# Optimization experiments

Hardware: AMD Instinct MI355X
Metric: run time of the kernel (lower is better)

The kernel has to match this reference:

```python
import jax, jax.numpy as jnp
import numpy as np

NUM_HEADS = 16
NEG_INF = -1e30


def setup_inputs() -> dict:
    key = jax.random.key(0)
    k1, k2, k3 = jax.random.split(key, 3)
    B, S, D = 2, 2048, 1024
    x = jax.random.normal(k1, (B, S, D), dtype=jnp.float32)
    # torch Linear(D, 3D, bias=False) stored here already transposed: y = x @ w_qkv
    w_qkv = jax.random.normal(k2, (D, 3 * D), dtype=jnp.float32) * 0.02
    w_out = jax.random.normal(k3, (D, D), dtype=jnp.float32) * 0.02
    return {"x": x, "w_qkv": w_qkv, "w_out": w_out}


def reference(x, w_qkv, w_out):
    B, S, D = x.shape
    H = NUM_HEADS
    dh = D // H
    qkv = x @ w_qkv                      # [B, S, 3D]
    q, k, v = jnp.split(qkv, 3, axis=-1)

    def to_heads(t):
        return t.reshape(B, S, H, dh).transpose(0, 2, 1, 3)  # [B, H, S, dh]

    q, k, v = to_heads(q), to_heads(k), to_heads(v)
    scale = jnp.asarray(dh, x.dtype) ** -0.5
    scores = jnp.einsum('bhqd,bhkd->bhqk', q, k) * scale     # [B, H, S, S]
    causal = jnp.tril(jnp.ones((S, S), dtype=bool))
    scores = jnp.where(causal, scores, NEG_INF)
    attn = jax.nn.softmax(scores, axis=-1)
    out = jnp.einsum('bhqk,bhkd->bhqd', attn, v)             # [B, H, S, dh]
    out = out.transpose(0, 2, 1, 3).reshape(B, S, D)
    return out @ w_out
```

## Files before the change

kernel.cpp:

```cpp
#include <hip/hip_runtime.h>

typedef unsigned short u16;
typedef unsigned int u32;

typedef __bf16 bf16x8 __attribute__((ext_vector_type(8)));
typedef _Float16 f16x8 __attribute__((ext_vector_type(8)));
typedef _Float16 f16x2 __attribute__((ext_vector_type(2)));
typedef float f32x4 __attribute__((ext_vector_type(4)));

typedef __attribute__((address_space(1))) u32 as1_u32;
typedef __attribute__((address_space(3))) u32 as3_u32;

__device__ __forceinline__ u16 f2bf(float x) {
  u32 u = __float_as_uint(x);
  u = u + 0x7fffu + ((u >> 16) & 1u);
  return (u16)(u >> 16);
}
__device__ __forceinline__ u32 pack2(float a, float b) {
  return (u32)f2bf(a) | ((u32)f2bf(b) << 16);
}
__device__ __forceinline__ u32 pkf16(float a, float b) {
  return __builtin_bit_cast(u32, __builtin_amdgcn_cvt_pkrtz(a, b));
}
__device__ __forceinline__ void gld_lds16(const u16* g, const u16* l) {
  __builtin_amdgcn_global_load_lds((const as1_u32*)g, (as3_u32*)l, 16, 0, 0);
}

__global__ void cvt_bf16_kernel(const float* __restrict__ in, u16* __restrict__ out, int n4) {
  int i = blockIdx.x * blockDim.x + threadIdx.x;
  if (i < n4) {
    float4 v = ((const float4*)in)[i];
    uint2 r;
    r.x = pack2(v.x, v.y);
    r.y = pack2(v.z, v.w);
    ((uint2*)out)[i] = r;
  }
}

__global__ __launch_bounds__(256) void transpose_bf16_tiled(const float* __restrict__ W,
                                                            u16* __restrict__ WT,
                                                            int K, int N) {
  __shared__ float tile[64][65];
  int k0 = blockIdx.x * 64, n0 = blockIdx.y * 64;
  int t = threadIdx.x;
  int r = t >> 4, c4 = (t & 15) * 4;
#pragma unroll
  for (int i = 0; i < 4; ++i) {
    int row = r + i * 16;
    float4 v = *(const float4*)&W[(size_t)(k0 + row) * N + n0 + c4];
    tile[row][c4 + 0] = v.x; tile[row][c4 + 1] = v.y;
    tile[row][c4 + 2] = v.z; tile[row][c4 + 3] = v.w;
  }
  __syncthreads();
#pragma unroll
  for (int i = 0; i < 4; ++i) {
    int n = r + i * 16;
    uint2 o;
    o.x = pack2(tile[c4 + 0][n], tile[c4 + 1][n]);
    o.y = pack2(tile[c4 + 2][n], tile[c4 + 3][n]);
    *(uint2*)&WT[(size_t)(n0 + n) * K + k0 + c4] = o;
  }
}

template <int OUT_MODE>
__global__ __launch_bounds__(256) void gemm_bt_kernel(const u16* __restrict__ A,
                                                      const u16* __restrict__ BT,
                                                      void* __restrict__ Cv,
                                                      u16* __restrict__ VT,
                                                      int M, int N, int K) {
  __shared__ __attribute__((aligned(16))) u16 sA[128 * 32];
  __shared__ __attribute__((aligned(16))) u16 sB[128 * 32];
  const int tid = threadIdx.x;
  const int wave = tid >> 6;
  const int lane = tid & 63;
  const int bm = blockIdx.y * 128;
  const int bn = blockIdx.x * 128;
  const int wm = (wave >> 1) * 64;
  const int wn = (wave & 1) * 64;
  const int lr = lane & 15;
  const int kg = lane >> 4;

  const int srow = tid >> 2;
  const int scol = (tid & 3) * 8;
  const u16* pa0 = A + (size_t)(bm + srow) * K + scol;
  const u16* pa1 = pa0 + (size_t)64 * K;
  const u16* pb0 = BT + (size_t)(bn + srow) * K + scol;
  const u16* pb1 = pb0 + (size_t)64 * K;
  const u16* la = sA + wave * 512;
  const u16* lb = sB + wave * 512;

  f32x4 acc[4][4];
#pragma unroll
  for (int i = 0; i < 4; i++)
#pragma unroll
    for (int j = 0; j < 4; j++) {
      f32x4 z = {0.f, 0.f, 0.f, 0.f};
      acc[i][j] = z;
    }

  for (int k0 = 0; k0 < K; k0 += 32) {
    __syncthreads();
    gld_lds16(pa0 + k0, la);
    gld_lds16(pa1 + k0, la + 2048);
    gld_lds16(pb0 + k0, lb);
    gld_lds16(pb1 + k0, lb + 2048);
    __syncthreads();
    bf16x8 af[4], bfr[4];
#pragma unroll
    for (int mi = 0; mi < 4; mi++)
      af[mi] = *(const bf16x8*)(sA + (wm + mi * 16 + lr) * 32 + kg * 8);
#pragma unroll
    for (int ni = 0; ni < 4; ni++)
      bfr[ni] = *(const bf16x8*)(sB + (wn + ni * 16 + lr) * 32 + kg * 8);
#pragma unroll
    for (int mi = 0; mi < 4; mi++)
#pragma unroll
      for (int ni = 0; ni < 4; ni++)
        acc[mi][ni] = __builtin_amdgcn_mfma_f32_16x16x32_bf16(af[mi], bfr[ni], acc[mi][ni], 0, 0, 0);
  }

#pragma unroll
  for (int mi = 0; mi < 4; mi++)
#pragma unroll
    for (int ni = 0; ni < 4; ni++) {
      int c = bn + wn + ni * 16 + lr;
      int r0 = bm + wm + mi * 16 + kg * 4;
      if (OUT_MODE == 0) {
#pragma unroll
        for (int rr = 0; rr < 4; rr++)
          ((float*)Cv)[(size_t)(r0 + rr) * N + c] = acc[mi][ni][rr];
      } else {
        if (c < 2048) {
          u16* qkp = (u16*)Cv;
#pragma unroll
          for (int rr = 0; rr < 4; rr++)
            qkp[(size_t)(r0 + rr) * 2048 + c] = f2bf(acc[mi][ni][rr]);
        } else {
          int cc = c - 2048;
          u32 lo = pkf16(acc[mi][ni][0], acc[mi][ni][1]);
          u32 hi = pkf16(acc[mi][ni][2], acc[mi][ni][3]);
          size_t vrow = ((size_t)(r0 >> 11) * 16 + (cc >> 6)) * 64 + (cc & 63);
          *(uint2*)(VT + vrow * 2048 + (r0 & 2047)) = make_uint2(lo, hi);
        }
      }
    }
}

__global__ __launch_bounds__(256) void attn_mfma_kernel(const u16* __restrict__ qk,
                                                        const u16* __restrict__ vt,
                                                        u16* __restrict__ out) {
  __shared__ __attribute__((aligned(16))) u16 sQ[2][64 * 32];
  __shared__ __attribute__((aligned(16))) u16 sK[2][64 * 32];
  __shared__ __attribute__((aligned(16))) u16 sV[2][64 * 32];
  __shared__ __attribute__((aligned(16))) u16 sP[4][16 * 72];

  const int tid = threadIdx.x;
  const int wave = tid >> 6;
  const int lane = tid & 63;
  const int lq = lane & 15;
  const int lg = lane >> 4;

  int idx = blockIdx.x;
  int qc = 31 - (idx >> 5);
  int bh = idx & 31;
  int b = bh >> 4, h = bh & 15;
  int q0 = qc * 64;

  const u16* qbase = qk + (size_t)b * 2048 * 2048 + h * 64;
  const u16* kbase = qbase + 1024;
  const u16* vbase = vt + (size_t)(b * 16 + h) * 64 * 2048;
  u16* obase = out + (size_t)b * 2048 * 1024 + h * 64;

  const int sreg = wave >> 1;
  const int srb = wave & 1;

#pragma unroll
  for (int it = 0; it < 2; ++it) {
    int rows0 = (srb * 2 + it) * 16;
    int row = rows0 + (lane >> 2);
    gld_lds16(qbase + (size_t)(q0 + row) * 2048 + sreg * 32 + (lane & 3) * 8,
              sQ[sreg] + rows0 * 32);
  }
  __syncthreads();

  bf16x8 qf0 = *(const bf16x8*)(sQ[0] + (wave * 16 + lq) * 32 + lg * 8);
  bf16x8 qf1 = *(const bf16x8*)(sQ[1] + (wave * 16 + lq) * 32 + lg * 8);

  float lsum = 0.f;
  f32x4 oacc[4];
#pragma unroll
  for (int i = 0; i < 4; ++i) {
    f32x4 z = {0.f, 0.f, 0.f, 0.f};
    oacc[i] = z;
  }

  const float EK = 0.18033688011112042f;
  u16* const pw = sP[wave] + lq * 72 + lg * 4;
  const u16* const pr = sP[wave] + lq * 72 + lg * 8;

  const int ntiles = qc + 1;
  for (int t = 0; t < ntiles; ++t) {
    int j0 = t * 64;
    __syncthreads();
#pragma unroll
    for (int it = 0; it < 2; ++it) {
      int rows0 = (srb * 2 + it) * 16;
      int row = rows0 + (lane >> 2);
      int coff = sreg * 32 + (lane & 3) * 8;
      gld_lds16(kbase + (size_t)(j0 + row) * 2048 + coff, sK[sreg] + rows0 * 32);
      gld_lds16(vbase + (size_t)row * 2048 + j0 + coff, sV[sreg] + rows0 * 32);
    }
    __syncthreads();

    if (t < qc) {
#pragma unroll
      for (int jt = 0; jt < 4; ++jt) {
        bf16x8 kf0 = *(const bf16x8*)(sK[0] + (jt * 16 + lq) * 32 + lg * 8);
        bf16x8 kf1 = *(const bf16x8*)(sK[1] + (jt * 16 + lq) * 32 + lg * 8);
        f32x4 c = {0.f, 0.f, 0.f, 0.f};
        c = __builtin_amdgcn_mfma_f32_16x16x32_bf16(kf0, qf0, c, 0, 0, 0);
        c = __builtin_amdgcn_mfma_f32_16x16x32_bf16(kf1, qf1, c, 0, 0, 0);
        float p0 = exp2f(c[0] * EK);
        float p1 = exp2f(c[1] * EK);
        float p2 = exp2f(c[2] * EK);
        float p3 = exp2f(c[3] * EK);
        lsum += (p0 + p1) + (p2 + p3);
        *(uint2*)(pw + jt * 16) = make_uint2(pkf16(p0, p1), pkf16(p2, p3));
      }
    } else {
#pragma unroll
      for (int jt = 0; jt < 4; ++jt) {
        if (jt <= wave) {
          bf16x8 kf0 = *(const bf16x8*)(sK[0] + (jt * 16 + lq) * 32 + lg * 8);
          bf16x8 kf1 = *(const bf16x8*)(sK[1] + (jt * 16 + lq) * 32 + lg * 8);
          f32x4 c = {0.f, 0.f, 0.f, 0.f};
          c = __builtin_amdgcn_mfma_f32_16x16x32_bf16(kf0, qf0, c, 0, 0, 0);
          c = __builtin_amdgcn_mfma_f32_16x16x32_bf16(kf1, qf1, c, 0, 0, 0);
          float p0 = exp2f(c[0] * EK);
          float p1 = exp2f(c[1] * EK);
          float p2 = exp2f(c[2] * EK);
          float p3 = exp2f(c[3] * EK);
          if (jt == wave) {
            int jr = lg * 4;
            p0 = (jr + 0 <= lq) ? p0 : 0.f;
            p1 = (jr + 1 <= lq) ? p1 : 0.f;
            p2 = (jr + 2 <= lq) ? p2 : 0.f;
            p3 = (jr + 3 <= lq) ? p3 : 0.f;
          }
          lsum += (p0 + p1) + (p2 + p3);
          *(uint2*)(pw + jt * 16) = make_uint2(pkf16(p0, p1), pkf16(p2, p3));
        } else {
          *(uint2*)(pw + jt * 16) = make_uint2(0u, 0u);
        }
      }
    }

    asm volatile("" ::: "memory");

    f16x8 pf0 = *(const f16x8*)(pr);
    f16x8 pf1 = *(const f16x8*)(pr + 32);
#pragma unroll
    for (int dt = 0; dt < 4; ++dt) {
      f16x8 vf0 = *(const f16x8*)(sV[0] + (dt * 16 + lq) * 32 + lg * 8);
      f16x8 vf1 = *(const f16x8*)(sV[1] + (dt * 16 + lq) * 32 + lg * 8);
      oacc[dt] = __builtin_amdgcn_mfma_f32_16x16x32_f16(vf0, pf0, oacc[dt], 0, 0, 0);
      oacc[dt] = __builtin_amdgcn_mfma_f32_16x16x32_f16(vf1, pf1, oacc[dt], 0, 0, 0);
    }
  }

  lsum += __shfl_xor(lsum, 16);
  lsum += __shfl_xor(lsum, 32);
  float inv = 1.0f / lsum;

#pragma unroll
  for (int dt = 0; dt < 4; ++dt) {
    int d = dt * 16 + lg * 4;
    u32 lo = pack2(oacc[dt][0] * inv, oacc[dt][1] * inv);
    u32 hi = pack2(oacc[dt][2] * inv, oacc[dt][3] * inv);
    *(uint2*)(obase + (size_t)(q0 + wave * 16 + lq) * 1024 + d) = make_uint2(lo, hi);
  }
}

extern "C" void kernel_launch(void* const* d_in, const int* in_sizes, int n_in,
                              void* d_out, int out_size, void* d_ws, size_t ws_size,
                              hipStream_t stream) {
  const float* x = (const float*)d_in[0];
  const float* w_qkv = (const float*)d_in[1];
  const float* w_out = (const float*)d_in[2];
  float* out = (float*)d_out;

  char* ws = (char*)d_ws;
  u16* xb    = (u16*)(ws);
  u16* wqkvT = (u16*)(ws + (8u << 20));
  u16* woutT = (u16*)(ws + (14u << 20));
  u16* qkb   = (u16*)(ws + (16u << 20));
  u16* vtb   = (u16*)(ws + (32u << 20));
  u16* attn  = (u16*)(ws + (40u << 20));

  cvt_bf16_kernel<<<4096, 256, 0, stream>>>(x, xb, 4194304 / 4);
  transpose_bf16_tiled<<<dim3(16, 48), 256, 0, stream>>>(w_qkv, wqkvT, 1024, 3072);
  transpose_bf16_tiled<<<dim3(16, 16), 256, 0, stream>>>(w_out, woutT, 1024, 1024);

  gemm_bt_kernel<2><<<dim3(3072 / 128, 4096 / 128), 256, 0, stream>>>(
      xb, wqkvT, (void*)qkb, vtb, 4096, 3072, 1024);

  attn_mfma_kernel<<<1024, 256, 0, stream>>>(qkb, vtb, attn);

  gemm_bt_kernel<0><<<dim3(1024 / 128, 4096 / 128), 256, 0, stream>>>(
      attn, woutT, (void*)out, nullptr, 4096, 1024, 1024);
}
```

Baseline: 193.3 us.

## Widen attention K/V tiles, fold softmax scale into Q, add V transpose pass

The attention loop now stages 128 keys per barrier pair instead of 64 and processes two 64-key subtiles per round, halving synchronisation and load rounds. The softmax scale is folded into Q in the QKV GEMM epilogue, removing a multiply per score. V is written row-major by the GEMM and transposed by a separate LDS kernel rather than through scattered strided stores. The output projection GEMM uses 64-wide N tiles to launch twice as many blocks. The extra kernel launch and the pass over V cost more memory traffic, and vtmp aliases the attn buffer.

```diff
diff --git a/kernel.cpp b/kernel.cpp
--- a/kernel.cpp
+++ b/kernel.cpp
@@ -5,11 +5,12 @@
 
 typedef __bf16 bf16x8 __attribute__((ext_vector_type(8)));
 typedef _Float16 f16x8 __attribute__((ext_vector_type(8)));
-typedef _Float16 f16x2 __attribute__((ext_vector_type(2)));
 typedef float f32x4 __attribute__((ext_vector_type(4)));
 
 typedef __attribute__((address_space(1))) u32 as1_u32;
 typedef __attribute__((address_space(3))) u32 as3_u32;
+
+#define EKF 0.18033688011112042f
 
 __device__ __forceinline__ u16 f2bf(float x) {
   u32 u = __float_as_uint(x);
@@ -21,6 +22,9 @@
 }
 __device__ __forceinline__ u32 pkf16(float a, float b) {
   return __builtin_bit_cast(u32, __builtin_amdgcn_cvt_pkrtz(a, b));
+}
+__device__ __forceinline__ u16 f2h(float a) {
+  return (u16)(pkf16(a, a) & 0xffffu);
 }
 __device__ __forceinline__ void gld_lds16(const u16* g, const u16* l) {
   __builtin_amdgcn_global_load_lds((const as1_u32*)g, (as3_u32*)l, 16, 0, 0);
@@ -62,21 +66,52 @@
   }
 }
 
-template <int OUT_MODE>
+__global__ __launch_bounds__(256) void transpose_vt_kernel(const u16* __restrict__ vtmp,
+                                                           u16* __restrict__ vt) {
+  __shared__ u16 t[64 * 71];
+  int j0 = blockIdx.x * 64;
+  int bh = blockIdx.y;
+  int b = bh >> 4, h = bh & 15;
+  int tid = threadIdx.x;
+  int r = tid >> 2, cs = (tid & 3) * 16;
+  const u16* src = vtmp + (size_t)(b * 2048 + j0 + r) * 1024 + h * 64 + cs;
+  uint4 a = ((const uint4*)src)[0];
+  uint4 c = ((const uint4*)src)[1];
+  u16* dst = &t[r * 71 + cs];
+  dst[0] = (u16)a.x; dst[1] = (u16)(a.x >> 16); dst[2] = (u16)a.y; dst[3] = (u16)(a.y >> 16);
+  dst[4] = (u16)a.z; dst[5] = (u16)(a.z >> 16); dst[6] = (u16)a.w; dst[7] = (u16)(a.w >> 16);
+  dst[8] = (u16)c.x; dst[9] = (u16)(c.x >> 16); dst[10] = (u16)c.y; dst[11] = (u16)(c.y >> 16);
+  dst[12] = (u16)c.z; dst[13] = (u16)(c.z >> 16); dst[14] = (u16)c.w; dst[15] = (u16)(c.w >> 16);
+  __syncthreads();
+  int d = tid >> 2, jseg = (tid & 3) * 16;
+  u32 w[8];
+#pragma unroll
+  for (int i = 0; i < 8; ++i) {
+    u32 lo = t[(jseg + 2 * i) * 71 + d];
+    u32 hi = t[(jseg + 2 * i + 1) * 71 + d];
+    w[i] = lo | (hi << 16);
+  }
+  u16* out = vt + (size_t)(bh * 64 + d) * 2048 + j0 + jseg;
+  ((uint4*)out)[0] = make_uint4(w[0], w[1], w[2], w[3]);
+  ((uint4*)out)[1] = make_uint4(w[4], w[5], w[6], w[7]);
+}
+
+template <int OUT_MODE, int BN>
 __global__ __launch_bounds__(256) void gemm_bt_kernel(const u16* __restrict__ A,
                                                       const u16* __restrict__ BT,
                                                       void* __restrict__ Cv,
                                                       u16* __restrict__ VT,
                                                       int M, int N, int K) {
+  const int NF = (BN == 128) ? 4 : 2;
   __shared__ __attribute__((aligned(16))) u16 sA[128 * 32];
-  __shared__ __attribute__((aligned(16))) u16 sB[128 * 32];
+  __shared__ __attribute__((aligned(16))) u16 sB[BN * 32];
   const int tid = threadIdx.x;
   const int wave = tid >> 6;
   const int lane = tid & 63;
   const int bm = blockIdx.y * 128;
-  const int bn = blockIdx.x * 128;
+  const int bn = blockIdx.x * BN;
   const int wm = (wave >> 1) * 64;
-  const int wn = (wave & 1) * 64;
+  const int wn = (wave & 1) * (BN / 2);
   const int lr = lane & 15;
   const int kg = lane >> 4;
 
@@ -89,11 +124,11 @@
   const u16* la = sA + wave * 512;
   const u16* lb = sB + wave * 512;
 
-  f32x4 acc[4][4];
+  f32x4 acc[4][NF];
 #pragma unroll
   for (int i = 0; i < 4; i++)
 #pragma unroll
-    for (int j = 0; j < 4; j++) {
+    for (int j = 0; j < NF; j++) {
       f32x4 z = {0.f, 0.f, 0.f, 0.f};
       acc[i][j] = z;
     }
@@ -103,26 +138,26 @@
     gld_lds16(pa0 + k0, la);
     gld_lds16(pa1 + k0, la + 2048);
     gld_lds16(pb0 + k0, lb);
-    gld_lds16(pb1 + k0, lb + 2048);
+    if (BN == 128) gld_lds16(pb1 + k0, lb + 2048);
     __syncthreads();
-    bf16x8 af[4], bfr[4];
+    bf16x8 af[4], bfr[NF];
 #pragma unroll
     for (int mi = 0; mi < 4; mi++)
       af[mi] = *(const bf16x8*)(sA + (wm + mi * 16 + lr) * 32 + kg * 8);
 #pragma unroll
-    for (int ni = 0; ni < 4; ni++)
+    for (int ni = 0; ni < NF; ni++)
       bfr[ni] = *(const bf16x8*)(sB + (wn + ni * 16 + lr) * 32 + kg * 8);
 #pragma unroll
     for (int mi = 0; mi < 4; mi++)
 #pragma unroll
-      for (int ni = 0; ni < 4; ni++)
+      for (int ni = 0; ni < NF; ni++)
         acc[mi][ni] = __builtin_amdgcn_mfma_f32_16x16x32_bf16(af[mi], bfr[ni], acc[mi][ni], 0, 0, 0);
   }
 
 #pragma unroll
   for (int mi = 0; mi < 4; mi++)
 #pragma unroll
-    for (int ni = 0; ni < 4; ni++) {
+    for (int ni = 0; ni < NF; ni++) {
       int c = bn + wn + ni * 16 + lr;
       int r0 = bm + wm + mi * 16 + kg * 4;
       if (OUT_MODE == 0) {
@@ -130,17 +165,21 @@
         for (int rr = 0; rr < 4; rr++)
           ((float*)Cv)[(size_t)(r0 + rr) * N + c] = acc[mi][ni][rr];
       } else {
-        if (c < 2048) {
+        if (c < 1024) {
+          u16* qkp = (u16*)Cv;
+#pragma unroll
+          for (int rr = 0; rr < 4; rr++)
+            qkp[(size_t)(r0 + rr) * 2048 + c] = f2bf(acc[mi][ni][rr] * EKF);
+        } else if (c < 2048) {
           u16* qkp = (u16*)Cv;
 #pragma unroll
           for (int rr = 0; rr < 4; rr++)
             qkp[(size_t)(r0 + rr) * 2048 + c] = f2bf(acc[mi][ni][rr]);
         } else {
           int cc = c - 2048;
-          u32 lo = pkf16(acc[mi][ni][0], acc[mi][ni][1]);
-          u32 hi = pkf16(acc[mi][ni][2], acc[mi][ni][3]);
-          size_t vrow = ((size_t)(r0 >> 11) * 16 + (cc >> 6)) * 64 + (cc & 63);
-          *(uint2*)(VT + vrow * 2048 + (r0 & 2047)) = make_uint2(lo, hi);
+#pragma unroll
+          for (int rr = 0; rr < 4; rr++)
+            VT[(size_t)(r0 + rr) * 1024 + cc] = f2h(acc[mi][ni][rr]);
         }
       }
     }
@@ -150,8 +189,8 @@
                                                         const u16* __restrict__ vt,
                                                         u16* __restrict__ out) {
   __shared__ __attribute__((aligned(16))) u16 sQ[2][64 * 32];
-  __shared__ __attribute__((aligned(16))) u16 sK[2][64 * 32];
-  __shared__ __attribute__((aligned(16))) u16 sV[2][64 * 32];
+  __shared__ __attribute__((aligned(16))) u16 sK[2][128 * 32];
+  __shared__ __attribute__((aligned(16))) u16 sV[4][64 * 32];
   __shared__ __attribute__((aligned(16))) u16 sP[4][16 * 72];
 
   const int tid = threadIdx.x;
@@ -168,18 +207,15 @@
 
   const u16* qbase = qk + (size_t)b * 2048 * 2048 + h * 64;
   const u16* kbase = qbase + 1024;
-  const u16* vbase = vt + (size_t)(b * 16 + h) * 64 * 2048;
+  const u16* vbase = vt + (size_t)bh * 64 * 2048;
   u16* obase = out + (size_t)b * 2048 * 1024 + h * 64;
 
-  const int sreg = wave >> 1;
-  const int srb = wave & 1;
-
 #pragma unroll
   for (int it = 0; it < 2; ++it) {
-    int rows0 = (srb * 2 + it) * 16;
+    int rows0 = ((wave & 1) * 2 + it) * 16;
     int row = rows0 + (lane >> 2);
-    gld_lds16(qbase + (size_t)(q0 + row) * 2048 + sreg * 32 + (lane & 3) * 8,
-              sQ[sreg] + rows0 * 32);
+    gld_lds16(qbase + (size_t)(q0 + row) * 2048 + (wave >> 1) * 32 + (lane & 3) * 8,
+              sQ[wave >> 1] + rows0 * 32);
   }
   __syncthreads();
 
@@ -194,77 +230,93 @@
     oacc[i] = z;
   }
 
-  const float EK = 0.18033688011112042f;
   u16* const pw = sP[wave] + lq * 72 + lg * 4;
   const u16* const pr = sP[wave] + lq * 72 + lg * 8;
-
-  const int ntiles = qc + 1;
-  for (int t = 0; t < ntiles; ++t) {
-    int j0 = t * 64;
+  const int wqmax = q0 + wave * 16 + 15;
+
+  const int rounds = (qc + 2) >> 1;
+  for (int r = 0; r < rounds; ++r) {
+    int j0 = r * 128;
     __syncthreads();
 #pragma unroll
-    for (int it = 0; it < 2; ++it) {
-      int rows0 = (srb * 2 + it) * 16;
+    for (int it = 0; it < 4; ++it) {
+      int rows0 = ((wave & 1) * 4 + it) * 16;
       int row = rows0 + (lane >> 2);
-      int coff = sreg * 32 + (lane & 3) * 8;
-      gld_lds16(kbase + (size_t)(j0 + row) * 2048 + coff, sK[sreg] + rows0 * 32);
-      gld_lds16(vbase + (size_t)row * 2048 + j0 + coff, sV[sreg] + rows0 * 32);
+      gld_lds16(kbase + (size_t)(j0 + row) * 2048 + (wave >> 1) * 32 + (lane & 3) * 8,
+                sK[wave >> 1] + rows0 * 32);
+    }
+#pragma unroll
+    for (int it = 0; it < 4; ++it) {
+      int rows0 = it * 16;
+      int drow = rows0 + (lane >> 2);
+      gld_lds16(vbase + (size_t)drow * 2048 + j0 + wave * 32 + (lane & 3) * 8,
+                sV[wave] + rows0 * 32);
     }
     __syncthreads();
 
-    if (t < qc) {
-#pragma unroll
-      for (int jt = 0; jt < 4; ++jt) {
-        bf16x8 kf0 = *(const bf16x8*)(sK[0] + (jt * 16 + lq) * 32 + lg * 8);
-        bf16x8 kf1 = *(const bf16x8*)(sK[1] + (jt * 16 + lq) * 32 + lg * 8);
-        f32x4 c = {0.f, 0.f, 0.f, 0.f};
-        c = __builtin_amdgcn_mfma_f32_16x16x32_bf16(kf0, qf0, c, 0, 0, 0);
-        c = __builtin_amdgcn_mfma_f32_16x16x32_bf16(kf1, qf1, c, 0, 0, 0);
-        float p0 = exp2f(c[0] * EK);
-        float p1 = exp2f(c[1] * EK);
-        float p2 = exp2f(c[2] * EK);
-        float p3 = exp2f(c[3] * EK);
-        lsum += (p0 + p1) + (p2 + p3);
-        *(uint2*)(pw + jt * 16) = make_uint2(pkf16(p0, p1), pkf16(p2, p3));
-      }
-    } else {
-#pragma unroll
-      for (int jt = 0; jt < 4; ++jt) {
-        if (jt <= wave) {
-          bf16x8 kf0 = *(const bf16x8*)(sK[0] + (jt * 16 + lq) * 32 + lg * 8);
-          bf16x8 kf1 = *(const bf16x8*)(sK[1] + (jt * 16 + lq) * 32 + lg * 8);
+#pragma unroll
+    for (int u = 0; u < 2; ++u) {
+      int js = j0 + u * 64;
+      if (js > wqmax) continue;
+      const u16* sKu = sK[0] + u * 64 * 32;
+      const u16* sKu1 = sK[1] + u * 64 * 32;
+
+      if (js < q0) {
+#pragma unroll
+        for (int jt = 0; jt < 4; ++jt) {
+          bf16x8 kf0 = *(const bf16x8*)(sKu + (jt * 16 + lq) * 32 + lg * 8);
+          bf16x8 kf1 = *(const bf16x8*)(sKu1 + (jt * 16 + lq) * 32 + lg * 8);
           f32x4 c = {0.f, 0.f, 0.f, 0.f};
           c = __builtin_amdgcn_mfma_f32_16x16x32_bf16(kf0, qf0, c, 0, 0, 0);
           c = __builtin_amdgcn_mfma_f32_16x16x32_bf16(kf1, qf1, c, 0, 0, 0);
-          float p0 = exp2f(c[0] * EK);
-          float p1 = exp2f(c[1] * EK);
-          float p2 = exp2f(c[2] * EK);
-          float p3 = exp2f(c[3] * EK);
-          if (jt == wave) {
-            int jr = lg * 4;
-            p0 = (jr + 0 <= lq) ? p0 : 0.f;
-            p1 = (jr + 1 <= lq) ? p1 : 0.f;
-            p2 = (jr + 2 <= lq) ? p2 : 0.f;
-            p3 = (jr + 3 <= lq) ? p3 : 0.f;
-          }
+          float p0 = exp2f(c[0]);
+          float p1 = exp2f(c[1]);
+          float p2 = exp2f(c[2]);
+          float p3 = exp2f(c[3]);
           lsum += (p0 + p1) + (p2 + p3);
           *(uint2*)(pw + jt * 16) = make_uint2(pkf16(p0, p1), pkf16(p2, p3));
-        } else {
-          *(uint2*)(pw + jt * 16) = make_uint2(0u, 0u);
+        }
+      } else {
+#pragma unroll
+        for (int jt = 0; jt < 4; ++jt) {
+          if (jt <= wave) {
+            bf16x8 kf0 = *(const bf16x8*)(sKu + (jt * 16 + lq) * 32 + lg * 8);
+            bf16x8 kf1 = *(const bf16x8*)(sKu1 + (jt * 16 + lq) * 32 + lg * 8);
+            f32x4 c = {0.f, 0.f, 0.f, 0.f};
+            c = __builtin_amdgcn_mfma_f32_16x16x32_bf16(kf0, qf0, c, 0, 0, 0);
+            c = __builtin_amdgcn_mfma_f32_16x16x32_bf16(kf1, qf1, c, 0, 0, 0);
+            float p0 = exp2f(c[0]);
+            float p1 = exp2f(c[1]);
+            float p2 = exp2f(c[2]);
+            float p3 = exp2f(c[3]);
+            if (jt == wave) {
+              int jr = lg * 4;
+              p0 = (jr + 0 <= lq) ? p0 : 0.f;
+              p1 = (jr + 1 <= lq) ? p1 : 0.f;
+              p2 = (jr + 2 <= lq) ? p2 : 0.f;
+              p3 = (jr + 3 <= lq) ? p3 : 0.f;
+            }
+            lsum += (p0 + p1) + (p2 + p3);
+            *(uint2*)(pw + jt * 16) = make_uint2(pkf16(p0, p1), pkf16(p2, p3));
+          } else {
+            *(uint2*)(pw + jt * 16) = make_uint2(0u, 0u);
+          }
         }
       }
-    }
-
-    asm volatile("" ::: "memory");
-
-    f16x8 pf0 = *(const f16x8*)(pr);
-    f16x8 pf1 = *(const f16x8*)(pr + 32);
-#pragma unroll
-    for (int dt = 0; dt < 4; ++dt) {
-      f16x8 vf0 = *(const f16x8*)(sV[0] + (dt * 16 + lq) * 32 + lg * 8);
-      f16x8 vf1 = *(const f16x8*)(sV[1] + (dt * 16 + lq) * 32 + lg * 8);
-      oacc[dt] = __builtin_amdgcn_mfma_f32_16x16x32_f16(vf0, pf0, oacc[dt], 0, 0, 0);
-      oacc[dt] = __builtin_amdgcn_mfma_f32_16x16x32_f16(vf1, pf1, oacc[dt], 0, 0, 0);
+
+      asm volatile("" ::: "memory");
+
+      f16x8 pf0 = *(const f16x8*)(pr);
+      f16x8 pf1 = *(const f16x8*)(pr + 32);
+      const u16* sVu = sV[u * 2];
+      const u16* sVu1 = sV[u * 2 + 1];
+#pragma unroll
+      for (int dt = 0; dt < 4; ++dt) {
+        f16x8 vf0 = *(const f16x8*)(sVu + (dt * 16 + lq) * 32 + lg * 8);
+        f16x8 vf1 = *(const f16x8*)(sVu1 + (dt * 16 + lq) * 32 + lg * 8);
+        oacc[dt] = __builtin_amdgcn_mfma_f32_16x16x32_f16(vf0, pf0, oacc[dt], 0, 0, 0);
+        oacc[dt] = __builtin_amdgcn_mfma_f32_16x16x32_f16(vf1, pf1, oacc[dt], 0, 0, 0);
+      }
     }
   }
 
@@ -295,17 +347,20 @@
   u16* woutT = (u16*)(ws + (14u << 20));
   u16* qkb   = (u16*)(ws + (16u << 20));
   u16* vtb   = (u16*)(ws + (32u << 20));
+  u16* vtmp  = (u16*)(ws + (40u << 20));
   u16* attn  = (u16*)(ws + (40u << 20));
 
   cvt_bf16_kernel<<<4096, 256, 0, stream>>>(x, xb, 4194304 / 4);
   transpose_bf16_tiled<<<dim3(16, 48), 256, 0, stream>>>(w_qkv, wqkvT, 1024, 3072);
   transpose_bf16_tiled<<<dim3(16, 16), 256, 0, stream>>>(w_out, woutT, 1024, 1024);
 
-  gemm_bt_kernel<2><<<dim3(3072 / 128, 4096 / 128), 256, 0, stream>>>(
-      xb, wqkvT, (void*)qkb, vtb, 4096, 3072, 1024);
+  gemm_bt_kernel<2, 128><<<dim3(3072 / 128, 4096 / 128), 256, 0, stream>>>(
+      xb, wqkvT, (void*)qkb, vtmp, 4096, 3072, 1024);
+
+  transpose_vt_kernel<<<dim3(32, 32), 256, 0, stream>>>(vtmp, vtb);
 
   attn_mfma_kernel<<<1024, 256, 0, stream>>>(qkb, vtb, attn);
 
-  gemm_bt_kernel<0><<<dim3(1024 / 128, 4096 / 128), 256, 0, stream>>>(
+  gemm_bt_kernel<0, 64><<<dim3(1024 / 64, 4096 / 128), 256, 0, stream>>>(
       attn, woutT, (void*)out, nullptr, 4096, 1024, 1024);
 }
```

New measurement: 194.2 us. Within noise of the previous version (+0.5%).
